# Optimization experiments

Hardware: AMD Instinct MI355X
Metric: run time of the kernel (lower is better)

## Reference

```python
import jax, jax.numpy as jnp
import numpy as np

D_MODEL = 2048
EXPAND = 2
INNER = EXPAND * D_MODEL          # 4096
HEADDIM = 64
NHEADS = INNER // HEADDIM         # 64
D_CONV = 4
BATCH, SEQLEN = 2, 4096


def setup_inputs() -> dict:
    key = jax.random.key(0)
    ks = jax.random.split(key, 12)
    f32 = jnp.float32
    return {
        "hidden_states": jax.random.normal(ks[0], (BATCH, SEQLEN, D_MODEL), f32),
        "in_proj_w": jax.random.normal(ks[1], (INNER, D_MODEL), f32) * 0.02,
        "gate_proj_w": jax.random.normal(ks[2], (INNER, D_MODEL), f32) * 0.02,
        "out_proj_w": jax.random.normal(ks[3], (D_MODEL, INNER), f32) * 0.02,
        "conv_weight": jax.random.normal(ks[4], (INNER, D_CONV), f32) * 0.02,
        "conv_bias": jnp.zeros((INNER,), f32),
        "dt_w": jax.random.normal(ks[5], (NHEADS, HEADDIM), f32) * 0.02,
        "dt_b": jnp.zeros((NHEADS,), f32),
        "A_log": jax.random.normal(ks[6], (NHEADS, HEADDIM), f32) * 0.1,
        "B": jax.random.normal(ks[7], (NHEADS, HEADDIM), f32) * 0.02,
        "C": jax.random.normal(ks[8], (NHEADS, HEADDIM), f32) * 0.02,
        "D": jnp.ones((NHEADS, HEADDIM), f32),
    }


def _dw_causal_conv_silu(x, w, b):
    # x: (B, L, C), w: (C, K), b: (C,). Causal depthwise conv + SiLU.
    K = w.shape[1]
    L = x.shape[1]
    xp = jnp.pad(x, ((0, 0), (K - 1, 0), (0, 0)))
    y = b
    for k in range(K):  # K=4, tiny fixed loop
        y = y + w[:, k] * xp[:, k:k + L, :]
    return jax.nn.silu(y)


def _diag_ssm_scan(a, u):
    # Linear recurrence s_t = a_t * s_{t-1} + u_t along axis=1 (seqlen).
    def comb(c1, c2):
        a1, b1 = c1
        a2, b2 = c2
        return a1 * a2, a2 * b1 + b2
    _, s = jax.lax.associative_scan(comb, (a, u), axis=1)
    return s


def reference(hidden_states, in_proj_w, gate_proj_w, out_proj_w,
              conv_weight, conv_bias, dt_w, dt_b, A_log, B, C, D):
    batch, seqlen, _ = hidden_states.shape
    projected = jnp.einsum('bld,cd->blc', hidden_states, in_proj_w)
    conv_out = _dw_causal_conv_silu(projected, conv_weight, conv_bias)
    gate = jax.nn.sigmoid(jnp.einsum('bld,cd->blc', hidden_states, gate_proj_w))

    X = conv_out.reshape(batch, seqlen, NHEADS, HEADDIM)
    dt = jax.nn.softplus(jnp.einsum('blhp,hp->blh', X, dt_w) + dt_b)  # (b,l,h)
    A = -jnp.exp(A_log)                                               # (h,p)

    a = jnp.exp(dt[..., None] * A)          # (b,l,h,p) decay factors
    u = dt[..., None] * B * X               # (b,l,h,p) driven input
    s = _diag_ssm_scan(a, u)                # (b,l,h,p) states
    y = C * s + D * X                       # (b,l,h,p)

    combined = y.reshape(batch, seqlen, INNER) * gate
    return jnp.einsum('blc,dc->bld', combined, out_proj_w)
```

## Files before the change

### kernel.cpp

```cpp
#include <hip/hip_runtime.h>
#include <cstdint>
#include <cstddef>

typedef unsigned short ushort;
typedef __attribute__((ext_vector_type(8))) short short8;
typedef __attribute__((ext_vector_type(8))) unsigned short ushort8;
typedef __attribute__((ext_vector_type(4))) float float4v;

#define DM    2048
#define INNERC 4096
#define LSEQ  4096
#define NBATCH 2
#define MROWS 8192
#define NHH   64
#define HDD   64
#define NCHUNK 32
#define CHLEN  128
#define CROWS 8

__device__ __forceinline__ float bf2f(ushort u) {
    return __uint_as_float(((unsigned int)u) << 16);
}
__device__ __forceinline__ ushort f2bf(float f) {
    unsigned int u = __float_as_uint(f);
    unsigned int r = u + 0x7FFFu + ((u >> 16) & 1u);
    return (ushort)(r >> 16);
}

__device__ __forceinline__ void async_cp16(const ushort* __restrict__ g, ushort* l) {
    __builtin_amdgcn_global_load_lds(
        (const __attribute__((address_space(1))) unsigned int*)g,
        (__attribute__((address_space(3))) unsigned int*)l,
        16, 0, 0);
}

__global__ void diag_kernel(float* __restrict__ out, float val) {
    if (threadIdx.x == 0 && blockIdx.x == 0) out[0] = val;
}

__global__ __launch_bounds__(256) void cast_bf16_kernel(
    const float* __restrict__ in, ushort* __restrict__ out, int n) {
    const int i = (blockIdx.x * 256 + threadIdx.x) * 8;
    if (i + 8 > n) return;
    const float4v a = *(const float4v*)(in + i);
    const float4v b = *(const float4v*)(in + i + 4);
    ushort8 o;
    o[0] = f2bf(a[0]); o[1] = f2bf(a[1]); o[2] = f2bf(a[2]); o[3] = f2bf(a[3]);
    o[4] = f2bf(b[0]); o[5] = f2bf(b[1]); o[6] = f2bf(b[2]); o[7] = f2bf(b[3]);
    *(ushort8*)(out + i) = o;
}

template <int EPI>
__global__ __launch_bounds__(256, 2) void gemm_bt(
    const ushort* __restrict__ Ab, const ushort* __restrict__ Wb,
    void* __restrict__ Out, const ushort* __restrict__ Aux,
    int M, int N, int K) {
    __shared__ ushort As[128 * 64];
    __shared__ ushort Bs[128 * 64];
    const int tid  = threadIdx.x;
    const int lane = tid & 63;
    const int w    = tid >> 6;
    const int wm   = w >> 1, wn = w & 1;
    const int row0 = blockIdx.y * 128;
    const int col0 = blockIdx.x * 128;

    float4v acc[4][4];
#pragma unroll
    for (int i = 0; i < 4; i++)
#pragma unroll
        for (int j = 0; j < 4; j++) {
            float4v z = {0.f, 0.f, 0.f, 0.f};
            acc[i][j] = z;
        }

    for (int k0 = 0; k0 < K; k0 += 64) {
        __syncthreads();
#pragma unroll
        for (int t = 0; t < 4; t++) {
            const int c   = t * 256 + tid;
            const int row = c >> 3;
            const int kg  = (c & 7) ^ (row & 7);
            async_cp16(Ab + (size_t)(row0 + row) * K + k0 + kg * 8, &As[c * 8]);
            async_cp16(Wb + (size_t)(col0 + row) * K + k0 + kg * 8, &Bs[c * 8]);
        }
        __syncthreads();
#pragma unroll
        for (int half = 0; half < 2; half++) {
            const int kq = half * 4 + (lane >> 4);
            short8 af[4], bfr[4];
#pragma unroll
            for (int rm = 0; rm < 4; rm++) {
                const int row = wm * 64 + rm * 16 + (lane & 15);
                af[rm] = *(const short8*)&As[(row * 8 + (kq ^ (row & 7))) * 8];
            }
#pragma unroll
            for (int cn = 0; cn < 4; cn++) {
                const int col = wn * 64 + cn * 16 + (lane & 15);
                bfr[cn] = *(const short8*)&Bs[(col * 8 + (kq ^ (col & 7))) * 8];
            }
#pragma unroll
            for (int rm = 0; rm < 4; rm++)
#pragma unroll
                for (int cn = 0; cn < 4; cn++)
                    acc[rm][cn] = __builtin_amdgcn_mfma_f32_16x16x32_bf16(
                        af[rm], bfr[cn], acc[rm][cn], 0, 0, 0);
        }
    }

#pragma unroll
    for (int rm = 0; rm < 4; rm++) {
#pragma unroll
        for (int cn = 0; cn < 4; cn++) {
            const int r0 = row0 + wm * 64 + rm * 16 + (lane >> 4) * 4;
            const int cc = col0 + wn * 64 + cn * 16 + (lane & 15);
#pragma unroll
            for (int rr = 0; rr < 4; rr++) {
                const float v   = acc[rm][cn][rr];
                const size_t off = (size_t)(r0 + rr) * N + cc;
                if (EPI == 0) {
                    ((ushort*)Out)[off] = f2bf(v);
                } else if (EPI == 1) {
                    const float g = 1.0f / (1.0f + __expf(-v));
                    ((ushort*)Out)[off] = f2bf(g * bf2f(Aux[off]));
                } else {
                    ((float*)Out)[off] = v;
                }
            }
        }
    }
}

__global__ __launch_bounds__(256) void conv_silu_kernel(
    const ushort* __restrict__ proj, const float* __restrict__ cw,
    const float* __restrict__ cb, ushort* __restrict__ X) {
    const int blk  = blockIdx.x;
    const int half = blk & 1;
    const int tile = blk >> 1;
    const int bl0  = tile * CROWS;
    const bool atStart = ((bl0 & (LSEQ - 1)) == 0);
    const int c0 = half * 2048 + threadIdx.x * 8;

    float4v w[8];
    const float4v* wp4 = (const float4v*)(cw + (size_t)c0 * 4);
#pragma unroll
    for (int t = 0; t < 8; t++) w[t] = wp4[t];
    float bias[8];
    const float4v b0 = *(const float4v*)(cb + c0);
    const float4v b1 = *(const float4v*)(cb + c0 + 4);
#pragma unroll
    for (int t = 0; t < 4; t++) { bias[t] = b0[t]; bias[t + 4] = b1[t]; }

    const size_t base = (size_t)bl0 * INNERC + c0;
    ushort8 w0, w1, w2;
    const ushort8 zz = {0, 0, 0, 0, 0, 0, 0, 0};
    if (atStart) {
        w0 = zz; w1 = zz; w2 = zz;
    } else {
        w0 = *(const ushort8*)(proj + base - 3 * (size_t)INNERC);
        w1 = *(const ushort8*)(proj + base - 2 * (size_t)INNERC);
        w2 = *(const ushort8*)(proj + base - 1 * (size_t)INNERC);
    }
#pragma unroll
    for (int r = 0; r < CROWS; r++) {
        const ushort8 cur = *(const ushort8*)(proj + base + (size_t)r * INNERC);
        ushort8 o;
#pragma unroll
        for (int j = 0; j < 8; j++) {
            const float acc = bias[j]
                + w[j][0] * bf2f(w0[j]) + w[j][1] * bf2f(w1[j])
                + w[j][2] * bf2f(w2[j]) + w[j][3] * bf2f(cur[j]);
            o[j] = f2bf(acc / (1.0f + __expf(-acc)));
        }
        *(ushort8*)(X + base + (size_t)r * INNERC) = o;
        w0 = w1; w1 = w2; w2 = cur;
    }
}

__global__ __launch_bounds__(64) void dt_kernel(
    const ushort* __restrict__ X, const float* __restrict__ dtw,
    const float* __restrict__ dtb, float* __restrict__ dt) {
    const int bl = blockIdx.x;
    const int h  = threadIdx.x;
    const ushort* xp = X + (size_t)bl * INNERC + h * 64;
    const float*  wp = dtw + h * 64;
    float acc = 0.0f;
#pragma unroll
    for (int p0 = 0; p0 < 64; p0 += 8) {
        const ushort8 xv = *(const ushort8*)(xp + p0);
#pragma unroll
        for (int j = 0; j < 8; j++) acc += bf2f(xv[j]) * wp[p0 + j];
    }
    const float z = acc + dtb[h];
    dt[bl * 64 + h] = (z > 20.0f) ? z : __logf(1.0f + __expf(z));
}

__global__ __launch_bounds__(256) void scan_pass1(
    const ushort* __restrict__ X, const float* __restrict__ dt,
    const float* __restrict__ A_log, const float* __restrict__ Bv,
    float* __restrict__ sumP, float* __restrict__ sumS) {
    const int task = blockIdx.x * 4 + (threadIdx.x >> 6);
    const int p  = threadIdx.x & 63;
    const int ch = task & (NCHUNK - 1);
    const int bh = task >> 5;
    const int h  = bh & 63;
    const int b  = bh >> 6;
    const float Ac = -__expf(A_log[h * 64 + p]);
    const float Bc = Bv[h * 64 + p];
    float Pr = 1.0f, s = 0.0f;
    const int bl0 = b * LSEQ + ch * CHLEN;
#pragma unroll 4
    for (int i = 0; i < CHLEN; i++) {
        const int bl   = bl0 + i;
        const float dtv = dt[bl * 64 + h];
        const float x   = bf2f(X[(size_t)bl * INNERC + h * 64 + p]);
        const float a   = __expf(dtv * Ac);
        Pr *= a;
        s = a * s + dtv * Bc * x;
    }
    sumP[(size_t)task * 64 + p] = Pr;
    sumS[(size_t)task * 64 + p] = s;
}

__global__ __launch_bounds__(64) void scan_pass2(
    const float* __restrict__ sumP, const float* __restrict__ sumS,
    float* __restrict__ carry) {
    const int bh = blockIdx.x;
    const int p  = threadIdx.x;
    float c = 0.0f;
    for (int ch = 0; ch < NCHUNK; ch++) {
        const size_t idx = ((size_t)bh * NCHUNK + ch) * 64 + p;
        carry[idx] = c;
        c = sumP[idx] * c + sumS[idx];
    }
}

__global__ __launch_bounds__(256) void scan_pass3(
    const ushort* __restrict__ X, const float* __restrict__ dt,
    const float* __restrict__ carry,
    const float* __restrict__ A_log, const float* __restrict__ Bv,
    const float* __restrict__ Cv, const float* __restrict__ Dv,
    ushort* __restrict__ Y) {
    const int task = blockIdx.x * 4 + (threadIdx.x >> 6);
    const int p  = threadIdx.x & 63;
    const int ch = task & (NCHUNK - 1);
    const int bh = task >> 5;
    const int h  = bh & 63;
    const int b  = bh >> 6;
    const float Ac = -__expf(A_log[h * 64 + p]);
    const float Bc = Bv[h * 64 + p];
    const float Cc = Cv[h * 64 + p];
    const float Dc = Dv[h * 64 + p];
    float s = carry[(size_t)task * 64 + p];
    const int bl0 = b * LSEQ + ch * CHLEN;
#pragma unroll 2
    for (int i = 0; i < CHLEN; i++) {
        const int bl = bl0 + i;
        const size_t xoff = (size_t)bl * INNERC + h * 64 + p;
        const float dtv = dt[bl * 64 + h];
        const float x   = bf2f(X[xoff]);
        const float a   = __expf(dtv * Ac);
        s = a * s + dtv * Bc * x;
        Y[xoff] = f2bf(Cc * s + Dc * x);
    }
}

#define OFF_PROJ  ((size_t)0)
#define OFF_HID   ((size_t)67108864)
#define OFF_WB    ((size_t)100663296)
#define OFF_DT    ((size_t)117440512)
#define OFF_SUMP  ((size_t)119537664)
#define OFF_SUMS  ((size_t)120586240)
#define OFF_CARRY ((size_t)121634816)
#define WS_NEEDED ((size_t)122683392)

extern "C" void kernel_launch(void* const* d_in, const int* in_sizes, int n_in,
                              void* d_out, int out_size, void* d_ws, size_t ws_size,
                              hipStream_t stream) {
    if (ws_size < WS_NEEDED) {
        diag_kernel<<<1, 64, 0, stream>>>((float*)d_out, (float)(ws_size >> 20));
        return;
    }
    const float* hidden = (const float*)d_in[0];
    const float* w_in   = (const float*)d_in[1];
    const float* w_gate = (const float*)d_in[2];
    const float* w_out  = (const float*)d_in[3];
    const float* conv_w = (const float*)d_in[4];
    const float* conv_b = (const float*)d_in[5];
    const float* dt_w   = (const float*)d_in[6];
    const float* dt_b   = (const float*)d_in[7];
    const float* A_log  = (const float*)d_in[8];
    const float* Bv     = (const float*)d_in[9];
    const float* Cv     = (const float*)d_in[10];
    const float* Dv     = (const float*)d_in[11];

    char* ws = (char*)d_ws;
    ushort* projbuf = (ushort*)(ws + OFF_PROJ);
    ushort* hid16   = (ushort*)(ws + OFF_HID);
    ushort* wbuf    = (ushort*)(ws + OFF_WB);
    float*  dtf     = (float*)(ws + OFF_DT);
    float*  sumP    = (float*)(ws + OFF_SUMP);
    float*  sumS    = (float*)(ws + OFF_SUMS);
    float*  carry   = (float*)(ws + OFF_CARRY);
    ushort* x16     = (ushort*)d_out;

    cast_bf16_kernel<<<8192, 256, 0, stream>>>(hidden, hid16, MROWS * DM);
    cast_bf16_kernel<<<4096, 256, 0, stream>>>(w_in, wbuf, INNERC * DM);

    gemm_bt<0><<<dim3(INNERC / 128, MROWS / 128), 256, 0, stream>>>(
        hid16, wbuf, projbuf, nullptr, MROWS, INNERC, DM);

    conv_silu_kernel<<<(MROWS / CROWS) * 2, 256, 0, stream>>>(projbuf, conv_w, conv_b, x16);
    dt_kernel<<<MROWS, 64, 0, stream>>>(x16, dt_w, dt_b, dtf);

    scan_pass1<<<(NBATCH * NHH * NCHUNK) / 4, 256, 0, stream>>>(
        x16, dtf, A_log, Bv, sumP, sumS);
    scan_pass2<<<NBATCH * NHH, 64, 0, stream>>>(sumP, sumS, carry);
    scan_pass3<<<(NBATCH * NHH * NCHUNK) / 4, 256, 0, stream>>>(
        x16, dtf, carry, A_log, Bv, Cv, Dv, projbuf);

    cast_bf16_kernel<<<4096, 256, 0, stream>>>(w_gate, wbuf, INNERC * DM);
    gemm_bt<1><<<dim3(INNERC / 128, MROWS / 128), 256, 0, stream>>>(
        hid16, wbuf, projbuf, projbuf, MROWS, INNERC, DM);

    cast_bf16_kernel<<<4096, 256, 0, stream>>>(w_out, wbuf, DM * INNERC);
    gemm_bt<2><<<dim3(DM / 128, MROWS / 128), 256, 0, stream>>>(
        projbuf, wbuf, d_out, nullptr, MROWS, DM, INNERC);
}
```

Before: 698.7 us.

## Fuse dt projection into conv, merge casts, remap GEMM blocks per XCD

Three changes. The dt projection is now computed inside the conv+SiLU kernel through per-head partial sums and shuffle reductions, which drops the separate dt kernel and its re-read of X. The hidden and in_proj weight casts are merged into one launch. GEMM blocks are remapped from a 1D grid so that each XCD (block index mod 8) takes a contiguous stripe of row tiles, aiming at better L2 reuse. The remap assumes M/128 is divisible by 8 and replaces the 2D grid.

New measurement: 721.4 us. +3.3%, slower.

```diff
diff --git a/kernel.cpp b/kernel.cpp
--- a/kernel.cpp
+++ b/kernel.cpp
@@ -39,15 +39,19 @@
 }
 
 __global__ __launch_bounds__(256) void cast_bf16_kernel(
-    const float* __restrict__ in, ushort* __restrict__ out, int n) {
-    const int i = (blockIdx.x * 256 + threadIdx.x) * 8;
-    if (i + 8 > n) return;
-    const float4v a = *(const float4v*)(in + i);
-    const float4v b = *(const float4v*)(in + i + 4);
+    const float* __restrict__ in, ushort* __restrict__ out, int nblk0,
+    const float* __restrict__ in2, ushort* __restrict__ out2) {
+    int b = blockIdx.x;
+    const float* src = in;
+    ushort* dst = out;
+    if (b >= nblk0) { b -= nblk0; src = in2; dst = out2; }
+    const int i = (b * 256 + threadIdx.x) * 8;
+    const float4v a = *(const float4v*)(src + i);
+    const float4v c = *(const float4v*)(src + i + 4);
     ushort8 o;
     o[0] = f2bf(a[0]); o[1] = f2bf(a[1]); o[2] = f2bf(a[2]); o[3] = f2bf(a[3]);
-    o[4] = f2bf(b[0]); o[5] = f2bf(b[1]); o[6] = f2bf(b[2]); o[7] = f2bf(b[3]);
-    *(ushort8*)(out + i) = o;
+    o[4] = f2bf(c[0]); o[5] = f2bf(c[1]); o[6] = f2bf(c[2]); o[7] = f2bf(c[3]);
+    *(ushort8*)(dst + i) = o;
 }
 
 template <int EPI>
@@ -61,8 +65,15 @@
     const int lane = tid & 63;
     const int w    = tid >> 6;
     const int wm   = w >> 1, wn = w & 1;
-    const int row0 = blockIdx.y * 128;
-    const int col0 = blockIdx.x * 128;
+
+    const int nbn    = N >> 7;
+    const int stripe = (M >> 7) >> 3;
+    const int xcd    = blockIdx.x & 7;
+    const int idx    = blockIdx.x >> 3;
+    const int bml    = idx / nbn;
+    const int bn     = idx - bml * nbn;
+    const int row0   = (xcd * stripe + bml) * 128;
+    const int col0   = bn * 128;
 
     float4v acc[4][4];
 #pragma unroll
@@ -132,7 +143,9 @@
 
 __global__ __launch_bounds__(256) void conv_silu_kernel(
     const ushort* __restrict__ proj, const float* __restrict__ cw,
-    const float* __restrict__ cb, ushort* __restrict__ X) {
+    const float* __restrict__ cb, const float* __restrict__ dtw,
+    const float* __restrict__ dtb,
+    ushort* __restrict__ X, float* __restrict__ dt) {
     const int blk  = blockIdx.x;
     const int half = blk & 1;
     const int tile = blk >> 1;
@@ -144,11 +157,18 @@
     const float4v* wp4 = (const float4v*)(cw + (size_t)c0 * 4);
 #pragma unroll
     for (int t = 0; t < 8; t++) w[t] = wp4[t];
-    float bias[8];
-    const float4v b0 = *(const float4v*)(cb + c0);
-    const float4v b1 = *(const float4v*)(cb + c0 + 4);
-#pragma unroll
-    for (int t = 0; t < 4; t++) { bias[t] = b0[t]; bias[t + 4] = b1[t]; }
+    float bias[8], dw[8];
+    {
+        const float4v b0 = *(const float4v*)(cb + c0);
+        const float4v b1 = *(const float4v*)(cb + c0 + 4);
+        const float4v d0 = *(const float4v*)(dtw + c0);
+        const float4v d1 = *(const float4v*)(dtw + c0 + 4);
+#pragma unroll
+        for (int t = 0; t < 4; t++) {
+            bias[t] = b0[t]; bias[t + 4] = b1[t];
+            dw[t] = d0[t]; dw[t + 4] = d1[t];
+        }
+    }
 
     const size_t base = (size_t)bl0 * INNERC + c0;
     ushort8 w0, w1, w2;
@@ -160,38 +180,37 @@
         w1 = *(const ushort8*)(proj + base - 2 * (size_t)INNERC);
         w2 = *(const ushort8*)(proj + base - 1 * (size_t)INNERC);
     }
+    float part[CROWS];
 #pragma unroll
     for (int r = 0; r < CROWS; r++) {
         const ushort8 cur = *(const ushort8*)(proj + base + (size_t)r * INNERC);
         ushort8 o;
+        float psum = 0.0f;
 #pragma unroll
         for (int j = 0; j < 8; j++) {
             const float acc = bias[j]
                 + w[j][0] * bf2f(w0[j]) + w[j][1] * bf2f(w1[j])
                 + w[j][2] * bf2f(w2[j]) + w[j][3] * bf2f(cur[j]);
-            o[j] = f2bf(acc / (1.0f + __expf(-acc)));
+            const float sx = acc / (1.0f + __expf(-acc));
+            o[j] = f2bf(sx);
+            psum += sx * dw[j];
         }
         *(ushort8*)(X + base + (size_t)r * INNERC) = o;
+        part[r] = psum;
         w0 = w1; w1 = w2; w2 = cur;
     }
-}
-
-__global__ __launch_bounds__(64) void dt_kernel(
-    const ushort* __restrict__ X, const float* __restrict__ dtw,
-    const float* __restrict__ dtb, float* __restrict__ dt) {
-    const int bl = blockIdx.x;
-    const int h  = threadIdx.x;
-    const ushort* xp = X + (size_t)bl * INNERC + h * 64;
-    const float*  wp = dtw + h * 64;
-    float acc = 0.0f;
-#pragma unroll
-    for (int p0 = 0; p0 < 64; p0 += 8) {
-        const ushort8 xv = *(const ushort8*)(xp + p0);
-#pragma unroll
-        for (int j = 0; j < 8; j++) acc += bf2f(xv[j]) * wp[p0 + j];
-    }
-    const float z = acc + dtb[h];
-    dt[bl * 64 + h] = (z > 20.0f) ? z : __logf(1.0f + __expf(z));
+#pragma unroll
+    for (int r = 0; r < CROWS; r++) {
+        float v = part[r];
+        v += __shfl_xor(v, 1);
+        v += __shfl_xor(v, 2);
+        v += __shfl_xor(v, 4);
+        if ((threadIdx.x & 7) == r) {
+            const int h = half * 32 + (threadIdx.x >> 3);
+            const float z = v + dtb[h];
+            dt[(bl0 + r) * 64 + h] = (z > 20.0f) ? z : __logf(1.0f + __expf(z));
+        }
+    }
 }
 
 __global__ __launch_bounds__(256) void scan_pass1(
@@ -303,14 +322,14 @@
     float*  carry   = (float*)(ws + OFF_CARRY);
     ushort* x16     = (ushort*)d_out;
 
-    cast_bf16_kernel<<<8192, 256, 0, stream>>>(hidden, hid16, MROWS * DM);
-    cast_bf16_kernel<<<4096, 256, 0, stream>>>(w_in, wbuf, INNERC * DM);
-
-    gemm_bt<0><<<dim3(INNERC / 128, MROWS / 128), 256, 0, stream>>>(
+    cast_bf16_kernel<<<8192 + 4096, 256, 0, stream>>>(
+        hidden, hid16, 8192, w_in, wbuf);
+
+    gemm_bt<0><<<(MROWS / 128) * (INNERC / 128), 256, 0, stream>>>(
         hid16, wbuf, projbuf, nullptr, MROWS, INNERC, DM);
 
-    conv_silu_kernel<<<(MROWS / CROWS) * 2, 256, 0, stream>>>(projbuf, conv_w, conv_b, x16);
-    dt_kernel<<<MROWS, 64, 0, stream>>>(x16, dt_w, dt_b, dtf);
+    conv_silu_kernel<<<(MROWS / CROWS) * 2, 256, 0, stream>>>(
+        projbuf, conv_w, conv_b, dt_w, dt_b, x16, dtf);
 
     scan_pass1<<<(NBATCH * NHH * NCHUNK) / 4, 256, 0, stream>>>(
         x16, dtf, A_log, Bv, sumP, sumS);
@@ -318,11 +337,11 @@
     scan_pass3<<<(NBATCH * NHH * NCHUNK) / 4, 256, 0, stream>>>(
         x16, dtf, carry, A_log, Bv, Cv, Dv, projbuf);
 
-    cast_bf16_kernel<<<4096, 256, 0, stream>>>(w_gate, wbuf, INNERC * DM);
-    gemm_bt<1><<<dim3(INNERC / 128, MROWS / 128), 256, 0, stream>>>(
+    cast_bf16_kernel<<<4096, 256, 0, stream>>>(w_gate, wbuf, 4096, nullptr, nullptr);
+    gemm_bt<1><<<(MROWS / 128) * (INNERC / 128), 256, 0, stream>>>(
         hid16, wbuf, projbuf, projbuf, MROWS, INNERC, DM);
 
-    cast_bf16_kernel<<<4096, 256, 0, stream>>>(w_out, wbuf, DM * INNERC);
-    gemm_bt<2><<<dim3(DM / 128, MROWS / 128), 256, 0, stream>>>(
+    cast_bf16_kernel<<<4096, 256, 0, stream>>>(w_out, wbuf, 4096, nullptr, nullptr);
+    gemm_bt<2><<<(MROWS / 128) * (DM / 128), 256, 0, stream>>>(
         projbuf, wbuf, d_out, nullptr, MROWS, DM, INNERC);
 }
```
